# Optimization experiments

Hardware: AMD Instinct MI355X
Metric: run time of the kernel (lower is better)

The kernel has to match this reference:

```python
import jax, jax.numpy as jnp
import numpy as np

B = 16384      # batch
FEAT = 4096    # features
D = 64         # nearest_root_factors(4096) -> (64, 64)
BN_EPS = 1e-3


def setup_inputs() -> dict:
    key = jax.random.key(0)
    ks = jax.random.split(key, 9)
    stdv1 = 1.0 / np.sqrt(D)   # layer1: zero_initialization=False path
    stdv2 = 0.001              # layer2: zero_initialization=True path

    def u(k, shape, s):
        return jax.random.uniform(k, shape, minval=-s, maxval=s, dtype=jnp.float32)

    return {
        "inputs": jax.random.normal(ks[0], (B, FEAT), dtype=jnp.float32),
        "bn0_gamma": jnp.ones((FEAT,), jnp.float32),
        "bn0_beta": jnp.zeros((FEAT,), jnp.float32),
        "bn1_gamma": jnp.ones((FEAT,), jnp.float32),
        "bn1_beta": jnp.zeros((FEAT,), jnp.float32),
        # Kronecker layer 1 (left: weights (o2=input_dim1, o1=out_dim1); right: (d,d))
        "k1_lw": u(ks[1], (D, D), stdv1),
        "k1_lb": u(ks[2], (D, D), stdv1),
        "k1_rw": u(ks[3], (D, D), stdv1),
        "k1_rb": u(ks[4], (D, D), stdv1),
        # Kronecker layer 2 (zero-initialized)
        "k2_lw": u(ks[5], (D, D), stdv2),
        "k2_lb": u(ks[6], (D, D), stdv2),
        "k2_rw": u(ks[7], (D, D), stdv2),
        "k2_rb": u(ks[8], (D, D), stdv2),
    }


def _batch_norm(x, gamma, beta):
    # training-mode BN: biased batch statistics over the batch dim, eps=1e-3
    m = jnp.mean(x, axis=0)
    v = jnp.var(x, axis=0)
    return (x - m) * jax.lax.rsqrt(v + BN_EPS) * gamma + beta


def _kron_block(t, lw, lb, rw, rb):
    # KDLeftLayer: permute(matmul(permute(x,[0,2,1]), W),[0,2,1]) + b
    #   out[b,o,j] = sum_k x[b,k,j] * W[k,o]
    t = jnp.einsum("bkj,ko->boj", t, lw) + lb
    # KDRightLayer: x @ W + b
    t = jnp.matmul(t, rw) + rb
    return t


def reference(inputs, bn0_gamma, bn0_beta, bn1_gamma, bn1_beta,
              k1_lw, k1_lb, k1_rw, k1_rb, k2_lw, k2_lb, k2_rw, k2_rb):
    t = jax.nn.relu(_batch_norm(inputs, bn0_gamma, bn0_beta))
    t = t.reshape(-1, D, D)
    t = _kron_block(t, k1_lw, k1_lb, k1_rw, k1_rb).reshape(-1, FEAT)
    t = jax.nn.relu(_batch_norm(t, bn1_gamma, bn1_beta))
    # dropout p=0.0 -> identity
    t = t.reshape(-1, D, D)
    t = _kron_block(t, k2_lw, k2_lb, k2_rw, k2_rb).reshape(-1, FEAT)
    return inputs + t
```

## Files before the change

kernel.cpp:

```cpp
#include <hip/hip_runtime.h>

#define NROWS 16384
#define NFEAT 4096

typedef __attribute__((ext_vector_type(8))) short          bfrag8;
typedef __attribute__((ext_vector_type(4))) float          fvec4;
typedef __attribute__((ext_vector_type(2))) float          fvec2;
typedef __attribute__((ext_vector_type(4))) unsigned short usvec4;
typedef __attribute__((ext_vector_type(8))) unsigned short usvec8;
typedef __attribute__((ext_vector_type(2))) unsigned int   uvec2;
typedef __attribute__((ext_vector_type(4))) unsigned int   uvec4;

#define WS_P0   ((size_t)0)
#define WS_P1   ((size_t)16 << 20)
#define WS_SC0  ((size_t)48 << 20)
#define WS_SH0  (WS_SC0 + 16384)
#define WS_SC1  (WS_SC0 + 32768)
#define WS_SH1  (WS_SC0 + 49152)
#define WS_C1P  (WS_SC0 + 65536)
#define WS_C2P  (WS_SC0 + 81920)
#define WS_T1   ((size_t)64 << 20)
#define WS_XB   ((size_t)192 << 20)
#define WS_XQ   ((size_t)320 << 20)

__device__ __forceinline__ unsigned short f2bf_bits(float f) {
  unsigned u = __builtin_bit_cast(unsigned, f);
  u += 0x7FFFu + ((u >> 16) & 1u);
  return (unsigned short)(u >> 16);
}
__device__ __forceinline__ float bf2f(unsigned short b) {
  return __builtin_bit_cast(float, ((unsigned)b) << 16);
}
__device__ __forceinline__ usvec4 pack4(fvec4 a) {
  usvec4 p;
#pragma unroll
  for (int e = 0; e < 4; ++e) p[e] = f2bf_bits(a[e]);
  return p;
}
__device__ __forceinline__ fvec4 unpack4(usvec4 p) {
  return fvec4{bf2f(p[0]), bf2f(p[1]), bf2f(p[2]), bf2f(p[3])};
}
__device__ __forceinline__ int swz64(int i) { return i ^ (((i >> 6) & 7) << 2); }
__device__ __forceinline__ void glds16(const void* g, void* l) {
  __builtin_amdgcn_global_load_lds(
      (const __attribute__((address_space(1))) void*)g,
      (__attribute__((address_space(3))) void*)l, 16, 0, 0);
}

__global__ __launch_bounds__(256) void k_bn0part(const float* __restrict__ x,
                                                 unsigned short* __restrict__ p0,
                                                 unsigned short* __restrict__ xb,
                                                 unsigned char* __restrict__ xq) {
  const int t = threadIdx.x, p = blockIdx.x;
  fvec4 s[4], sq[4];
#pragma unroll
  for (int q = 0; q < 4; ++q) { s[q] = fvec4{0.f,0.f,0.f,0.f}; sq[q] = s[q]; }
  for (int r = p * 16; r < p * 16 + 16; ++r) {
    const fvec4* row = (const fvec4*)(x + (size_t)r * NFEAT);
    usvec4* xrow = (usvec4*)(xb + (size_t)r * NFEAT);
#pragma unroll
    for (int q = 0; q < 4; ++q) {
      fvec4 v = row[t + 256 * q];
      s[q] += v; sq[q] += v * v;
      xrow[t + 256 * q] = pack4(v);
      int pq = __builtin_amdgcn_cvt_pk_fp8_f32(v[0], v[1], 0, false);
      pq     = __builtin_amdgcn_cvt_pk_fp8_f32(v[2], v[3], pq, true);
      *(unsigned*)(xq + (size_t)r * NFEAT + (t + 256 * q) * 4) = (unsigned)pq;
    }
  }
#pragma unroll
  for (int q = 0; q < 4; ++q) {
    int f0 = (t + 256 * q) * 4;
    *(usvec4*)(p0 + (size_t)p * 8192 + f0)        = pack4(s[q]);
    *(usvec4*)(p0 + (size_t)p * 8192 + 4096 + f0) = pack4(sq[q]);
  }
}

__device__ __forceinline__ void red_body(fvec4 (*red)[16][2],
                                         const unsigned short* __restrict__ parts,
                                         int nsets,
                                         const float* __restrict__ g,
                                         const float* __restrict__ bta,
                                         float* __restrict__ sc_out,
                                         float* __restrict__ sh_out, int j) {
  const int t = threadIdx.x;
  const int fc = t & 15, c = t >> 4;
  const int v = j * 64 + fc * 4;
  fvec4 s = fvec4{0.f,0.f,0.f,0.f}, q = s;
  for (int i = c; i < nsets; i += 16) {
    s += unpack4(*(const usvec4*)(parts + (size_t)i * 8192 + v));
    q += unpack4(*(const usvec4*)(parts + (size_t)i * 8192 + 4096 + v));
  }
  red[c][fc][0] = s; red[c][fc][1] = q;
  __syncthreads();
  if (c == 0) {
    fvec4 S = red[0][fc][0], Q = red[0][fc][1];
#pragma unroll
    for (int k = 1; k < 16; ++k) { S += red[k][fc][0]; Q += red[k][fc][1]; }
    fvec4 SC, SH;
    const float inv = 1.0f / NROWS;
#pragma unroll
    for (int e = 0; e < 4; ++e) {
      float mean = S[e] * inv;
      float var  = Q[e] * inv - mean * mean;
      float scv  = g[v + e] * rsqrtf(var + 1e-3f);
      SC[e] = scv; SH[e] = bta[v + e] - mean * scv;
    }
    *(fvec4*)(sc_out + v) = SC;
    *(fvec4*)(sh_out + v) = SH;
  }
}

__global__ __launch_bounds__(256) void k_prep0(const unsigned short* __restrict__ p0,
                                               const float* __restrict__ g0,
                                               const float* __restrict__ b0,
                                               float* __restrict__ sc0,
                                               float* __restrict__ sh0,
                                               const float* __restrict__ lb1,
                                               const float* __restrict__ rw1,
                                               const float* __restrict__ rb1,
                                               const float* __restrict__ lb2,
                                               const float* __restrict__ rw2,
                                               const float* __restrict__ rb2,
                                               unsigned* __restrict__ c1p,
                                               unsigned* __restrict__ c2p) {
  __shared__ fvec4 red[16][16][2];
  __shared__ float shc[256];
  if (blockIdx.x < 64) {
    red_body(red, p0, 1024, g0, b0, sc0, sh0, blockIdx.x);
  } else {
    const int bb   = blockIdx.x - 64;
    const int idx  = (bb & 15) * 256 + threadIdx.x;
    const int part = bb >> 4;
    const float* lb = part ? lb2 : lb1;
    const float* rw = part ? rw2 : rw1;
    const float* rb = part ? rb2 : rb1;
    int r = idx >> 6, o = idx & 63;
    float acc = rb[o * 64 + r];
    for (int j = 0; j < 64; ++j) acc += lb[o * 64 + j] * rw[j * 64 + r];
    shc[threadIdx.x] = acc;
    __syncthreads();
    if (!(idx & 64)) {
      float accO = shc[threadIdx.x ^ 64];
      unsigned pk = (unsigned)f2bf_bits(acc) | ((unsigned)f2bf_bits(accO) << 16);
      (part ? c2p : c1p)[o * 32 + (r >> 1)] = pk;
    }
  }
}

__global__ __launch_bounds__(256) void k_bn1stat(const unsigned char* __restrict__ t1q,
                                                 unsigned short* __restrict__ p1) {
  const int t = threadIdx.x, p = blockIdx.x;
  float s[16], q[16];
#pragma unroll
  for (int i = 0; i < 16; ++i) { s[i] = 0.f; q[i] = 0.f; }
  for (int r = p * 16; r < p * 16 + 16; ++r) {
    uvec4 v = *(const uvec4*)(t1q + (size_t)r * NFEAT + t * 16);
#pragma unroll
    for (int d = 0; d < 4; ++d) {
      fvec2 lo = __builtin_amdgcn_cvt_pk_f32_fp8((int)v[d], false);
      fvec2 hi = __builtin_amdgcn_cvt_pk_f32_fp8((int)v[d], true);
      float e0 = lo[0], e1 = lo[1], e2 = hi[0], e3 = hi[1];
      s[d*4+0] += e0; q[d*4+0] += e0*e0;
      s[d*4+1] += e1; q[d*4+1] += e1*e1;
      s[d*4+2] += e2; q[d*4+2] += e2*e2;
      s[d*4+3] += e3; q[d*4+3] += e3*e3;
    }
  }
#pragma unroll
  for (int b4 = 0; b4 < 4; ++b4) {
    fvec4 sv{s[b4*4], s[b4*4+1], s[b4*4+2], s[b4*4+3]};
    fvec4 qv{q[b4*4], q[b4*4+1], q[b4*4+2], q[b4*4+3]};
    *(usvec4*)(p1 + (size_t)p * 8192 + t * 16 + b4 * 4)        = pack4(sv);
    *(usvec4*)(p1 + (size_t)p * 8192 + 4096 + t * 16 + b4 * 4) = pack4(qv);
  }
}

__global__ __launch_bounds__(256) void k_red1(const unsigned short* __restrict__ p1,
                                              const float* __restrict__ g1,
                                              const float* __restrict__ b1,
                                              float* __restrict__ sc1,
                                              float* __restrict__ sh1) {
  __shared__ fvec4 red[16][16][2];
  red_body(red, p1, 1024, g1, b1, sc1, sh1, blockIdx.x);
}

template <int LAYER>
__global__ __launch_bounds__(256, 2) void k_kron(const unsigned char* __restrict__ aq,
                                                 const unsigned short* __restrict__ xbr,
                                                 const float* __restrict__ lw,
                                                 const float* __restrict__ rw,
                                                 const float* __restrict__ scv,
                                                 const float* __restrict__ shv,
                                                 const unsigned* __restrict__ cnp,
                                                 unsigned char* __restrict__ t1w,
                                                 float* __restrict__ outf) {
  __shared__ __align__(16) unsigned char  ldsA[4][2][4096];
  __shared__ __align__(16) unsigned short vt[4][4096];
  __shared__ __align__(16) unsigned scsh[4096];
  const int tid = threadIdx.x, bid = blockIdx.x;
  const int w = tid >> 6, l = tid & 63, m = l & 15, g = l >> 4;
  unsigned short* vtw = &vt[w][0];
  const int r0w = bid * 32 + w * 8;

#pragma unroll
  for (int c = 0; c < 16; ++c) {
    int f = tid * 16 + c;
    scsh[swz64(f)] = (unsigned)f2bf_bits(scv[f]) | ((unsigned)f2bf_bits(shv[f]) << 16);
  }
#pragma unroll
  for (int c = 0; c < 8; ++c)
    *(uvec4*)((char*)vtw + l * 128 + c * 16) = uvec4{0u, 0u, 0u, 0u};

  {
    const unsigned char* rb = aq + (size_t)r0w * NFEAT;
#pragma unroll
    for (int c = 0; c < 4; ++c)
      glds16(rb + c * 1024 + l * 16, &ldsA[w][0][c * 1024]);
  }

  bfrag8 frw[4][2];
#pragma unroll
  for (int rt = 0; rt < 4; ++rt)
#pragma unroll
    for (int ks = 0; ks < 2; ++ks)
#pragma unroll
      for (int i = 0; i < 8; ++i)
        frw[rt][ks][i] = (short)f2bf_bits(rw[(ks * 32 + g * 8 + i) * 64 + rt * 16 + m]);

  bfrag8 flw[4][2];
#pragma unroll
  for (int ot = 0; ot < 4; ++ot)
#pragma unroll
    for (int ks = 0; ks < 2; ++ks)
#pragma unroll
      for (int i = 0; i < 8; ++i)
        flw[ot][ks][i] = (short)f2bf_bits(lw[(ks * 32 + g * 8 + i) * 64 + ot * 16 + m]);

  uvec2 cbv[16];
#pragma unroll
  for (int rt2 = 0; rt2 < 4; ++rt2)
#pragma unroll
    for (int ot = 0; ot < 4; ++ot)
      cbv[rt2 * 4 + ot] = *(const uvec2*)(cnp + (ot * 16 + m) * 32 + rt2 * 8 + g * 2);

  __syncthreads();

#pragma unroll 1
  for (int rr = 0; rr < 8; ++rr) {
    const int rrow = r0w + rr;
    const unsigned char* A = &ldsA[w][rr & 1][0];

    asm volatile("s_waitcnt vmcnt(0)");

    usvec4 res[16];
    if constexpr (LAYER == 2) {
#pragma unroll
      for (int ot = 0; ot < 4; ++ot)
#pragma unroll
        for (int rt2 = 0; rt2 < 4; ++rt2)
          res[ot * 4 + rt2] = *(const usvec4*)(xbr + (size_t)rrow * NFEAT +
                                               (ot * 16 + m) * 64 + rt2 * 16 + g * 4);
    }

#pragma unroll
    for (int kt = 0; kt < 4; ++kt) {
      bfrag8 fa[2];
#pragma unroll
      for (int ks = 0; ks < 2; ++ks) {
        int f0 = (kt * 16 + m) * 64 + ks * 32 + g * 8;
        uvec4 c0  = *(const uvec4*)&scsh[swz64(f0)];
        uvec4 c1v = *(const uvec4*)&scsh[swz64(f0 + 4)];
        uvec2 tv = *(const uvec2*)(A + (kt * 16 + m) * 64 + ks * 32 + g * 8);
        fvec2 d0 = __builtin_amdgcn_cvt_pk_f32_fp8((int)tv[0], false);
        fvec2 d1 = __builtin_amdgcn_cvt_pk_f32_fp8((int)tv[0], true);
        fvec2 d2 = __builtin_amdgcn_cvt_pk_f32_fp8((int)tv[1], false);
        fvec2 d3 = __builtin_amdgcn_cvt_pk_f32_fp8((int)tv[1], true);
        float xs[8] = {d0[0], d0[1], d1[0], d1[1], d2[0], d2[1], d3[0], d3[1]};
        usvec8 u;
#pragma unroll
        for (int i = 0; i < 8; ++i) {
          unsigned dw = (i < 4) ? c0[i] : c1v[i - 4];
          float scf = __builtin_bit_cast(float, dw << 16);
          float shf = __builtin_bit_cast(float, dw & 0xffff0000u);
          u[i] = f2bf_bits(fmaxf(fmaf(xs[i], scf, shf), 0.f));
        }
        fa[ks] = __builtin_bit_cast(bfrag8, u);
      }
#pragma unroll
      for (int rt = 0; rt < 4; ++rt) {
        fvec4 va = fvec4{0.f, 0.f, 0.f, 0.f};
        va = __builtin_amdgcn_mfma_f32_16x16x32_bf16(fa[0], frw[rt][0], va, 0, 0, 0);
        va = __builtin_amdgcn_mfma_f32_16x16x32_bf16(fa[1], frw[rt][1], va, 0, 0, 0);
        int ridx = rt * 16 + m;
        int chunk = 2 * kt + (g >> 1);
        int byte = ridx * 128 + ((chunk ^ (ridx & 7)) << 4) + (g & 1) * 8;
        *(usvec4*)((char*)vtw + byte) = pack4(va);
      }
    }

    asm volatile("s_waitcnt lgkmcnt(0)");

    if (rr + 1 < 8) {
      const unsigned char* rb = aq + (size_t)(rrow + 1) * NFEAT;
#pragma unroll
      for (int c = 0; c < 4; ++c)
        glds16(rb + c * 1024 + l * 16, &ldsA[w][(rr + 1) & 1][c * 1024]);
    }

#pragma unroll
    for (int rt2 = 0; rt2 < 4; ++rt2) {
      int ridx = rt2 * 16 + m;
      bfrag8 a0 = __builtin_bit_cast(bfrag8, *(const usvec8*)((const char*)vtw +
                    ridx * 128 + (((0 + g) ^ (ridx & 7)) << 4)));
      bfrag8 a1 = __builtin_bit_cast(bfrag8, *(const usvec8*)((const char*)vtw +
                    ridx * 128 + (((4 + g) ^ (ridx & 7)) << 4)));
      fvec4 acc[4];
#pragma unroll
      for (int ot = 0; ot < 4; ++ot) {
        acc[ot] = fvec4{0.f, 0.f, 0.f, 0.f};
        acc[ot] = __builtin_amdgcn_mfma_f32_16x16x32_bf16(a0, flw[ot][0], acc[ot], 0, 0, 0);
        acc[ot] = __builtin_amdgcn_mfma_f32_16x16x32_bf16(a1, flw[ot][1], acc[ot], 0, 0, 0);
      }
#pragma unroll
      for (int ot = 0; ot < 4; ++ot) {
        uvec2 cv = cbv[rt2 * 4 + ot];
        fvec4 cb4{__builtin_bit_cast(float, cv[0] << 16),
                  __builtin_bit_cast(float, cv[0] & 0xffff0000u),
                  __builtin_bit_cast(float, cv[1] << 16),
                  __builtin_bit_cast(float, cv[1] & 0xffff0000u)};
        fvec4 z = acc[ot] + cb4;
        int foff = (ot * 16 + m) * 64 + rt2 * 16 + g * 4;
        if constexpr (LAYER == 1) {
          int pq = __builtin_amdgcn_cvt_pk_fp8_f32(z[0], z[1], 0, false);
          pq     = __builtin_amdgcn_cvt_pk_fp8_f32(z[2], z[3], pq, true);
          *(unsigned*)(t1w + (size_t)rrow * NFEAT + foff) = (unsigned)pq;
        } else {
          *(fvec4*)(outf + (size_t)rrow * NFEAT + foff) =
              unpack4(res[ot * 4 + rt2]) + z;
        }
      }
    }
  }
}

extern "C" void kernel_launch(void* const* d_in, const int* in_sizes, int n_in,
                              void* d_out, int out_size, void* d_ws, size_t ws_size,
                              hipStream_t stream) {
  (void)in_sizes; (void)n_in; (void)out_size; (void)ws_size;
  const float* x    = (const float*)d_in[0];
  const float* g0   = (const float*)d_in[1];
  const float* b0   = (const float*)d_in[2];
  const float* g1   = (const float*)d_in[3];
  const float* b1   = (const float*)d_in[4];
  const float* k1lw = (const float*)d_in[5];
  const float* k1lb = (const float*)d_in[6];
  const float* k1rw = (const float*)d_in[7];
  const float* k1rb = (const float*)d_in[8];
  const float* k2lw = (const float*)d_in[9];
  const float* k2lb = (const float*)d_in[10];
  const float* k2rw = (const float*)d_in[11];
  const float* k2rb = (const float*)d_in[12];
  char* ws = (char*)d_ws;

  unsigned short* p0  = (unsigned short*)(ws + WS_P0);
  unsigned short* p1  = (unsigned short*)(ws + WS_P1);
  unsigned char*  t1q = (unsigned char*)(ws + WS_T1);
  unsigned short* xb  = (unsigned short*)(ws + WS_XB);
  unsigned char*  xq  = (unsigned char*)(ws + WS_XQ);
  float* sc0 = (float*)(ws + WS_SC0);
  float* sh0 = (float*)(ws + WS_SH0);
  float* sc1 = (float*)(ws + WS_SC1);
  float* sh1 = (float*)(ws + WS_SH1);
  unsigned* c1p = (unsigned*)(ws + WS_C1P);
  unsigned* c2p = (unsigned*)(ws + WS_C2P);

  k_bn0part<<<1024, 256, 0, stream>>>(x, p0, xb, xq);
  k_prep0<<<96, 256, 0, stream>>>(p0, g0, b0, sc0, sh0,
                                  k1lb, k1rw, k1rb, k2lb, k2rw, k2rb, c1p, c2p);
  k_kron<1><<<512, 256, 0, stream>>>(xq, nullptr, k1lw, k1rw, sc0, sh0, c1p,
                                     t1q, nullptr);
  k_bn1stat<<<1024, 256, 0, stream>>>(t1q, p1);
  k_red1<<<64, 256, 0, stream>>>(p1, g1, b1, sc1, sh1);
  k_kron<2><<<512, 256, 0, stream>>>(t1q, xb, k2lw, k2rw, sc1, sh1, c2p,
                                     nullptr, (float*)d_out);
}
```

Baseline: 336.0 us.

## Drop bf16 residual copy, read fp32 input directly, register-prefetch fp8 rows

Removes the bf16 copy of the input written by the BN0 stats kernel. The second Kronecker layer now reads the fp32 residual straight from the original input, so one 128MB write and a 128MB read are gone but 256MB of fp32 is read instead. The LDS double buffer filled with global_load_lds is replaced by a register double-buffer that prefetches the next row's fp8 fragments. s_setprio is added around the MFMA section to favour compute waves.

After: 405.9 us. 1.21x slower.

```diff
diff --git a/kernel.cpp b/kernel.cpp
--- a/kernel.cpp
+++ b/kernel.cpp
@@ -20,8 +20,7 @@
 #define WS_C1P  (WS_SC0 + 65536)
 #define WS_C2P  (WS_SC0 + 81920)
 #define WS_T1   ((size_t)64 << 20)
-#define WS_XB   ((size_t)192 << 20)
-#define WS_XQ   ((size_t)320 << 20)
+#define WS_XQ   ((size_t)192 << 20)
 
 __device__ __forceinline__ unsigned short f2bf_bits(float f) {
   unsigned u = __builtin_bit_cast(unsigned, f);
@@ -41,15 +40,9 @@
   return fvec4{bf2f(p[0]), bf2f(p[1]), bf2f(p[2]), bf2f(p[3])};
 }
 __device__ __forceinline__ int swz64(int i) { return i ^ (((i >> 6) & 7) << 2); }
-__device__ __forceinline__ void glds16(const void* g, void* l) {
-  __builtin_amdgcn_global_load_lds(
-      (const __attribute__((address_space(1))) void*)g,
-      (__attribute__((address_space(3))) void*)l, 16, 0, 0);
-}
 
 __global__ __launch_bounds__(256) void k_bn0part(const float* __restrict__ x,
                                                  unsigned short* __restrict__ p0,
-                                                 unsigned short* __restrict__ xb,
                                                  unsigned char* __restrict__ xq) {
   const int t = threadIdx.x, p = blockIdx.x;
   fvec4 s[4], sq[4];
@@ -57,12 +50,10 @@
   for (int q = 0; q < 4; ++q) { s[q] = fvec4{0.f,0.f,0.f,0.f}; sq[q] = s[q]; }
   for (int r = p * 16; r < p * 16 + 16; ++r) {
     const fvec4* row = (const fvec4*)(x + (size_t)r * NFEAT);
-    usvec4* xrow = (usvec4*)(xb + (size_t)r * NFEAT);
 #pragma unroll
     for (int q = 0; q < 4; ++q) {
       fvec4 v = row[t + 256 * q];
       s[q] += v; sq[q] += v * v;
-      xrow[t + 256 * q] = pack4(v);
       int pq = __builtin_amdgcn_cvt_pk_fp8_f32(v[0], v[1], 0, false);
       pq     = __builtin_amdgcn_cvt_pk_fp8_f32(v[2], v[3], pq, true);
       *(unsigned*)(xq + (size_t)r * NFEAT + (t + 256 * q) * 4) = (unsigned)pq;
@@ -187,7 +178,7 @@
 
 template <int LAYER>
 __global__ __launch_bounds__(256, 2) void k_kron(const unsigned char* __restrict__ aq,
-                                                 const unsigned short* __restrict__ xbr,
+                                                 const float* __restrict__ xres,
                                                  const float* __restrict__ lw,
                                                  const float* __restrict__ rw,
                                                  const float* __restrict__ scv,
@@ -195,13 +186,11 @@
                                                  const unsigned* __restrict__ cnp,
                                                  unsigned char* __restrict__ t1w,
                                                  float* __restrict__ outf) {
-  __shared__ __align__(16) unsigned char  ldsA[4][2][4096];
   __shared__ __align__(16) unsigned short vt[4][4096];
   __shared__ __align__(16) unsigned scsh[4096];
   const int tid = threadIdx.x, bid = blockIdx.x;
   const int w = tid >> 6, l = tid & 63, m = l & 15, g = l >> 4;
   unsigned short* vtw = &vt[w][0];
-  const int r0w = bid * 32 + w * 8;
 
 #pragma unroll
   for (int c = 0; c < 16; ++c) {
@@ -212,13 +201,6 @@
   for (int c = 0; c < 8; ++c)
     *(uvec4*)((char*)vtw + l * 128 + c * 16) = uvec4{0u, 0u, 0u, 0u};
 
-  {
-    const unsigned char* rb = aq + (size_t)r0w * NFEAT;
-#pragma unroll
-    for (int c = 0; c < 4; ++c)
-      glds16(rb + c * 1024 + l * 16, &ldsA[w][0][c * 1024]);
-  }
-
   bfrag8 frw[4][2];
 #pragma unroll
   for (int rt = 0; rt < 4; ++rt)
@@ -246,22 +228,38 @@
 
   __syncthreads();
 
-#pragma unroll 1
-  for (int rr = 0; rr < 8; ++rr) {
-    const int rrow = r0w + rr;
-    const unsigned char* A = &ldsA[w][rr & 1][0];
-
-    asm volatile("s_waitcnt vmcnt(0)");
-
-    usvec4 res[16];
+  const int r0w = bid * 32 + w * 8;
+
+  uvec2 sQ0[8], sQ1[8];
+  {
+    const uvec2* p = (const uvec2*)(aq + (size_t)r0w * NFEAT);
+#pragma unroll
+    for (int kt = 0; kt < 4; ++kt)
+#pragma unroll
+      for (int ks = 0; ks < 2; ++ks)
+        sQ0[kt * 2 + ks] = p[(kt * 16 + m) * 8 + ks * 4 + g];
+  }
+
+  auto row_body = [&](int rrow, uvec2 (&curQ)[8], uvec2 (&nxtQ)[8], bool pf) {
+    if (pf) {
+      const uvec2* p = (const uvec2*)(aq + (size_t)(rrow + 1) * NFEAT);
+#pragma unroll
+      for (int kt = 0; kt < 4; ++kt)
+#pragma unroll
+        for (int ks = 0; ks < 2; ++ks)
+          nxtQ[kt * 2 + ks] = p[(kt * 16 + m) * 8 + ks * 4 + g];
+    }
+    fvec4 res[16];
     if constexpr (LAYER == 2) {
 #pragma unroll
       for (int ot = 0; ot < 4; ++ot)
 #pragma unroll
         for (int rt2 = 0; rt2 < 4; ++rt2)
-          res[ot * 4 + rt2] = *(const usvec4*)(xbr + (size_t)rrow * NFEAT +
-                                               (ot * 16 + m) * 64 + rt2 * 16 + g * 4);
-    }
+          res[ot * 4 + rt2] = *(const fvec4*)(xres + (size_t)rrow * NFEAT +
+                                              (ot * 16 + m) * 64 + rt2 * 16 + g * 4);
+    }
+
+    __builtin_amdgcn_s_setprio(1);
 
 #pragma unroll
     for (int kt = 0; kt < 4; ++kt) {
@@ -271,7 +269,7 @@
         int f0 = (kt * 16 + m) * 64 + ks * 32 + g * 8;
         uvec4 c0  = *(const uvec4*)&scsh[swz64(f0)];
         uvec4 c1v = *(const uvec4*)&scsh[swz64(f0 + 4)];
-        uvec2 tv = *(const uvec2*)(A + (kt * 16 + m) * 64 + ks * 32 + g * 8);
+        uvec2 tv = curQ[kt * 2 + ks];
         fvec2 d0 = __builtin_amdgcn_cvt_pk_f32_fp8((int)tv[0], false);
         fvec2 d1 = __builtin_amdgcn_cvt_pk_f32_fp8((int)tv[0], true);
         fvec2 d2 = __builtin_amdgcn_cvt_pk_f32_fp8((int)tv[1], false);
@@ -301,13 +299,6 @@
 
     asm volatile("s_waitcnt lgkmcnt(0)");
 
-    if (rr + 1 < 8) {
-      const unsigned char* rb = aq + (size_t)(rrow + 1) * NFEAT;
-#pragma unroll
-      for (int c = 0; c < 4; ++c)
-        glds16(rb + c * 1024 + l * 16, &ldsA[w][(rr + 1) & 1][c * 1024]);
-    }
-
 #pragma unroll
     for (int rt2 = 0; rt2 < 4; ++rt2) {
       int ridx = rt2 * 16 + m;
@@ -322,6 +313,7 @@
         acc[ot] = __builtin_amdgcn_mfma_f32_16x16x32_bf16(a0, flw[ot][0], acc[ot], 0, 0, 0);
         acc[ot] = __builtin_amdgcn_mfma_f32_16x16x32_bf16(a1, flw[ot][1], acc[ot], 0, 0, 0);
       }
+      if (rt2 == 3) __builtin_amdgcn_s_setprio(0);
 #pragma unroll
       for (int ot = 0; ot < 4; ++ot) {
         uvec2 cv = cbv[rt2 * 4 + ot];
@@ -336,11 +328,15 @@
           pq     = __builtin_amdgcn_cvt_pk_fp8_f32(z[2], z[3], pq, true);
           *(unsigned*)(t1w + (size_t)rrow * NFEAT + foff) = (unsigned)pq;
         } else {
-          *(fvec4*)(outf + (size_t)rrow * NFEAT + foff) =
-              unpack4(res[ot * 4 + rt2]) + z;
+          *(fvec4*)(outf + (size_t)rrow * NFEAT + foff) = res[ot * 4 + rt2] + z;
         }
       }
     }
+  };
+
+  for (int rp = 0; rp < 4; ++rp) {
+    row_body(r0w + 2 * rp,     sQ0, sQ1, true);
+    row_body(r0w + 2 * rp + 1, sQ1, sQ0, rp < 3);
   }
 }
 
@@ -366,7 +362,6 @@
   unsigned short* p0  = (unsigned short*)(ws + WS_P0);
   unsigned short* p1  = (unsigned short*)(ws + WS_P1);
   unsigned char*  t1q = (unsigned char*)(ws + WS_T1);
-  unsigned short* xb  = (unsigned short*)(ws + WS_XB);
   unsigned char*  xq  = (unsigned char*)(ws + WS_XQ);
   float* sc0 = (float*)(ws + WS_SC0);
   float* sh0 = (float*)(ws + WS_SH0);
@@ -375,13 +370,13 @@
   unsigned* c1p = (unsigned*)(ws + WS_C1P);
   unsigned* c2p = (unsigned*)(ws + WS_C2P);
 
-  k_bn0part<<<1024, 256, 0, stream>>>(x, p0, xb, xq);
+  k_bn0part<<<1024, 256, 0, stream>>>(x, p0, xq);
   k_prep0<<<96, 256, 0, stream>>>(p0, g0, b0, sc0, sh0,
                                   k1lb, k1rw, k1rb, k2lb, k2rw, k2rb, c1p, c2p);
   k_kron<1><<<512, 256, 0, stream>>>(xq, nullptr, k1lw, k1rw, sc0, sh0, c1p,
                                      t1q, nullptr);
   k_bn1stat<<<1024, 256, 0, stream>>>(t1q, p1);
   k_red1<<<64, 256, 0, stream>>>(p1, g1, b1, sc1, sh1);
-  k_kron<2><<<512, 256, 0, stream>>>(t1q, xb, k2lw, k2rw, sc1, sh1, c2p,
+  k_kron<2><<<512, 256, 0, stream>>>(t1q, x, k2lw, k2rw, sc1, sh1, c2p,
                                      nullptr, (float*)d_out);
 }
```
